# Performance work log

Measured on AMD Instinct MI355X. Metric: run time of the kernel, lower is better.

The kernel has to match this reference:

```python
import jax, jax.numpy as jnp
import numpy as np

D = 2048
N_DRUG, N_PROT = 10000, 20000
E = 100000


def setup_inputs() -> dict:
    key = jax.random.key(0)
    ks = jax.random.split(key, 10)
    return {
        "x_drug": jax.random.normal(ks[0], (N_DRUG, D), dtype=jnp.float32),
        "x_protein": jax.random.normal(ks[1], (N_PROT, D), dtype=jnp.float32),
        "rel_ddi": jax.random.normal(ks[2], (D,), dtype=jnp.float32),
        "rel_dpi": jax.random.normal(ks[3], (D,), dtype=jnp.float32),
        "ddi_src": jax.random.randint(ks[4], (E,), 0, N_DRUG, dtype=jnp.int64 if jax.config.jax_enable_x64 else jnp.int32),
        "ddi_dst": jax.random.randint(ks[5], (E,), 0, N_DRUG, dtype=jnp.int64 if jax.config.jax_enable_x64 else jnp.int32),
        "dpi_src": jax.random.randint(ks[6], (E,), 0, N_DRUG, dtype=jnp.int64 if jax.config.jax_enable_x64 else jnp.int32),
        "dpi_dst": jax.random.randint(ks[7], (E,), 0, N_PROT, dtype=jnp.int64 if jax.config.jax_enable_x64 else jnp.int32),
        "ppi_src": jax.random.randint(ks[8], (E,), 0, N_PROT, dtype=jnp.int64 if jax.config.jax_enable_x64 else jnp.int32),
        "ppi_dst": jax.random.randint(ks[9], (E,), 0, N_PROT, dtype=jnp.int64 if jax.config.jax_enable_x64 else jnp.int32),
    }


def _edge_score(x_src, x_dst, src, dst, rel):
    # gather [E, D] head/tail, DistMult-style multiply-reduce, clamp to [0, 1]
    head = x_src[src]
    tail = x_dst[dst]
    score = jnp.sum(head * rel * tail, axis=-1)
    return jnp.clip(score, 0.0, 1.0)


def reference(x_drug, x_protein, rel_ddi, rel_dpi,
              ddi_src, ddi_dst, dpi_src, dpi_dst, ppi_src, ppi_dst):
    score_ddi = _edge_score(x_drug, x_drug, ddi_src, ddi_dst, rel_ddi)
    score_dpi = _edge_score(x_drug, x_protein, dpi_src, dpi_dst, rel_dpi)
    # NOTE: original module (faithfully) applies the DPI relation to PPI edges
    score_ppi = _edge_score(x_protein, x_protein, ppi_src, ppi_dst, rel_dpi)
    return (score_ddi, score_dpi, score_ppi)
```

## Files before the change

kernel.cpp:

```cpp
#include <hip/hip_runtime.h>

#define D4 512
#define K_EDGES 32


__global__ void zero_ints(int* __restrict__ p, int n) {
    int i = blockIdx.x * blockDim.x + threadIdx.x;
    if (i < n) p[i] = 0;
}

__global__ void hist3(const int* __restrict__ s0, const int* __restrict__ s1,
                      const int* __restrict__ s2, int E,
                      int* __restrict__ cnt, int O1, int O2) {
    int i = blockIdx.x * blockDim.x + threadIdx.x;
    const int total = 3 * E;
    for (; i < total; i += gridDim.x * blockDim.x) {
        if (i < E)           atomicAdd(&cnt[s0[i]], 1);
        else if (i < 2 * E)  atomicAdd(&cnt[O1 + s1[i - E]], 1);
        else                 atomicAdd(&cnt[O2 + s2[i - 2 * E]], 1);
    }
}

__global__ void alloc3(const int* __restrict__ cnt, int* __restrict__ base,
                       int* __restrict__ cursors, int O1, int O2, int CBp) {
    int i = blockIdx.x * blockDim.x + threadIdx.x;
    if (i >= CBp) return;
    const int lane = threadIdx.x & 63;
    const int rel = (i >= O2) ? 2 : (i >= O1) ? 1 : 0;
    int c = cnt[i];
    int x = c;
#pragma unroll
    for (int d = 1; d < 64; d <<= 1) {
        int y = __shfl_up(x, d, 64);
        if (lane >= d) x += y;
    }
    int tot = __shfl(x, 63);
    int wb = 0;
    if (lane == 63) wb = atomicAdd(&cursors[rel], tot);
    wb = __shfl(wb, 63);
    base[i] = wb + x - c;
}

__global__ void scatter3(const int* __restrict__ s0, const int* __restrict__ d0_,
                         const int* __restrict__ s1, const int* __restrict__ d1_,
                         const int* __restrict__ s2, const int* __restrict__ d2_,
                         int E, int* __restrict__ base, int O1, int O2,
                         int* __restrict__ sorted, int* __restrict__ sd) {
    int i = blockIdx.x * blockDim.x + threadIdx.x;
    const int total = 3 * E;
    for (; i < total; i += gridDim.x * blockDim.x) {
        if (i < E) {
            int s = s0[i], d = d0_[i];
            int p = atomicAdd(&base[s], 1);
            sorted[p] = i; sd[p] = (s << 16) | d;
        } else if (i < 2 * E) {
            int k = i - E; int s = s1[k], d = d1_[k];
            int p = atomicAdd(&base[O1 + s], 1);
            sorted[E + p] = k; sd[E + p] = (s << 16) | d;
        } else {
            int k = i - 2 * E; int s = s2[k], d = d2_[k];
            int p = atomicAdd(&base[O2 + s], 1);
            sorted[2 * E + p] = k; sd[2 * E + p] = (s << 16) | d;
        }
    }
}

__global__ __launch_bounds__(256, 4) void score_sorted(
    const float4* __restrict__ xdrug, const float4* __restrict__ xprot,
    const float4* __restrict__ rddi,  const float4* __restrict__ rdpi,
    const int* __restrict__ sorted, const int* __restrict__ sd,
    int* __restrict__ queue, float* __restrict__ out, int E)
{
    const int lane = threadIdx.x & 63;
    const int wpb = blockDim.x >> 6;
    const int wid = blockIdx.x * wpb + (threadIdx.x >> 6);
    const int nw = gridDim.x * wpb;
    const int cpr = (E + K_EDGES - 1) / K_EDGES;
    const int total_chunks = 3 * cpr;

    int c = wid;
    while (c < total_chunks) {
        const int r = (c >= 2 * cpr) ? 2 : (c >= cpr) ? 1 : 0;
        const int ci = c - r * cpr;
        const int e_lo = ci * K_EDGES;
        const int n = min(K_EDGES, E - e_lo);

        const float4 *xs, *xd, *rel;
        if (r == 0)      { xs = xdrug; xd = xdrug; rel = rddi; }
        else if (r == 1) { xs = xdrug; xd = xprot; rel = rdpi; }
        else             { xs = xprot; xd = xprot; rel = rdpi; }
        const int* sl  = sorted + (size_t)r * E + e_lo;
        const int* sdl = sd     + (size_t)r * E + e_lo;
        float* o = out + (size_t)r * E;

        int eL = 0, sdL = 0;
        if (lane < n) { eL = sl[lane]; sdL = sdl[lane]; }

        float4 hr[8], tA[8], tB[8];
        int cur = -1;

        {
            int sd0 = __shfl(sdL, 0);
            const float4* tp = xd + (size_t)(sd0 & 0xffff) * D4;
#pragma unroll
            for (int j = 0; j < 8; ++j) tA[j] = tp[j * 64 + lane];
        }

        for (int i = 0; i < n; i += 2) {
            if (i + 1 < n) {
                int sdn = __shfl(sdL, i + 1);
                const float4* tq = xd + (size_t)(sdn & 0xffff) * D4;
#pragma unroll
                for (int j = 0; j < 8; ++j) tB[j] = tq[j * 64 + lane];
            }
            {
                int sdi = __shfl(sdL, i);
                int s = sdi >> 16;
                if (s != cur) {
                    cur = s;
                    const float4* hp = xs + (size_t)s * D4;
#pragma unroll
                    for (int j = 0; j < 8; ++j) {
                        float4 h = hp[j * 64 + lane], rv = rel[j * 64 + lane];
                        hr[j].x = h.x * rv.x; hr[j].y = h.y * rv.y;
                        hr[j].z = h.z * rv.z; hr[j].w = h.w * rv.w;
                    }
                }
                float acc = 0.f;
#pragma unroll
                for (int j = 0; j < 8; ++j) {
                    acc = fmaf(hr[j].x, tA[j].x, acc);
                    acc = fmaf(hr[j].y, tA[j].y, acc);
                    acc = fmaf(hr[j].z, tA[j].z, acc);
                    acc = fmaf(hr[j].w, tA[j].w, acc);
                }
#pragma unroll
                for (int off = 32; off; off >>= 1) acc += __shfl_down(acc, off, 64);
                int e = __shfl(eL, i);
                if (lane == 0) o[e] = fminf(fmaxf(acc, 0.f), 1.f);
            }
            if (i + 1 >= n) break;
            if (i + 2 < n) {
                int sdn = __shfl(sdL, i + 2);
                const float4* tq = xd + (size_t)(sdn & 0xffff) * D4;
#pragma unroll
                for (int j = 0; j < 8; ++j) tA[j] = tq[j * 64 + lane];
            }
            {
                int sdi = __shfl(sdL, i + 1);
                int s = sdi >> 16;
                if (s != cur) {
                    cur = s;
                    const float4* hp = xs + (size_t)s * D4;
#pragma unroll
                    for (int j = 0; j < 8; ++j) {
                        float4 h = hp[j * 64 + lane], rv = rel[j * 64 + lane];
                        hr[j].x = h.x * rv.x; hr[j].y = h.y * rv.y;
                        hr[j].z = h.z * rv.z; hr[j].w = h.w * rv.w;
                    }
                }
                float acc = 0.f;
#pragma unroll
                for (int j = 0; j < 8; ++j) {
                    acc = fmaf(hr[j].x, tB[j].x, acc);
                    acc = fmaf(hr[j].y, tB[j].y, acc);
                    acc = fmaf(hr[j].z, tB[j].z, acc);
                    acc = fmaf(hr[j].w, tB[j].w, acc);
                }
#pragma unroll
                for (int off = 32; off; off >>= 1) acc += __shfl_down(acc, off, 64);
                int e = __shfl(eL, i + 1);
                if (lane == 0) o[e] = fminf(fmaxf(acc, 0.f), 1.f);
            }
        }

        int nc = 0;
        if (lane == 0) nc = atomicAdd(queue, 1);
        c = nw + __shfl(nc, 0);
    }
}

__global__ __launch_bounds__(256) void edge_score_all(
    const float4* __restrict__ xdrug, const float4* __restrict__ xprot,
    const float4* __restrict__ rddi,  const float4* __restrict__ rdpi,
    const int* __restrict__ ddi_src, const int* __restrict__ ddi_dst,
    const int* __restrict__ dpi_src, const int* __restrict__ dpi_dst,
    const int* __restrict__ ppi_src, const int* __restrict__ ppi_dst,
    float* __restrict__ out, int E)
{
    __shared__ float4 srel[2][D4];
    for (int i = threadIdx.x; i < D4; i += blockDim.x) {
        srel[0][i] = rddi[i];
        srel[1][i] = rdpi[i];
    }
    __syncthreads();
    const int lane = threadIdx.x & 63;
    const int wpb = blockDim.x >> 6;
    int wid = blockIdx.x * wpb + (threadIdx.x >> 6);
    const int nw = gridDim.x * wpb;
    const int total = 3 * E;
    for (int e = wid; e < total; e += nw) {
        const float4 *hp, *tp;
        int sel;
        if (e < E)          { hp = xdrug + (size_t)ddi_src[e] * D4; tp = xdrug + (size_t)ddi_dst[e] * D4; sel = 0; }
        else if (e < 2 * E) { int k = e - E;     hp = xdrug + (size_t)dpi_src[k] * D4; tp = xprot + (size_t)dpi_dst[k] * D4; sel = 1; }
        else                { int k = e - 2 * E; hp = xprot + (size_t)ppi_src[k] * D4; tp = xprot + (size_t)ppi_dst[k] * D4; sel = 1; }
        float acc = 0.f;
#pragma unroll
        for (int j = 0; j < 8; ++j) {
            const int idx = j * 64 + lane;
            float4 h = hp[idx], t = tp[idx], rr = srel[sel][idx];
            acc = fmaf(h.x * rr.x, t.x, acc);
            acc = fmaf(h.y * rr.y, t.y, acc);
            acc = fmaf(h.z * rr.z, t.z, acc);
            acc = fmaf(h.w * rr.w, t.w, acc);
        }
#pragma unroll
        for (int off = 32; off; off >>= 1) acc += __shfl_down(acc, off, 64);
        if (lane == 0) out[e] = fminf(fmaxf(acc, 0.f), 1.f);
    }
}

extern "C" void kernel_launch(void* const* d_in, const int* in_sizes, int n_in,
                              void* d_out, int out_size, void* d_ws, size_t ws_size,
                              hipStream_t stream) {
    const float* x_drug    = (const float*)d_in[0];
    const float* x_protein = (const float*)d_in[1];
    const float* rel_ddi   = (const float*)d_in[2];
    const float* rel_dpi   = (const float*)d_in[3];
    const int* ddi_src = (const int*)d_in[4];
    const int* ddi_dst = (const int*)d_in[5];
    const int* dpi_src = (const int*)d_in[6];
    const int* dpi_dst = (const int*)d_in[7];
    const int* ppi_src = (const int*)d_in[8];
    const int* ppi_dst = (const int*)d_in[9];

    const int D  = in_sizes[2];
    const int nd = in_sizes[0] / D;
    const int np = in_sizes[1] / D;
    const int E  = in_sizes[4];
    float* out = (float*)d_out;

    const int ndp = ((nd + 63) / 64) * 64;
    const int npp = ((np + 63) / 64) * 64;
    const int O1  = ndp;
    const int O2  = ndp + ndp;
    const int CBp = O2 + npp;

    const size_t need = (size_t)(2 * CBp + 8 + 6 * E) * sizeof(int);

    if (ws_size < need) {
        edge_score_all<<<2048, 256, 0, stream>>>(
            (const float4*)x_drug, (const float4*)x_protein,
            (const float4*)rel_ddi, (const float4*)rel_dpi,
            ddi_src, ddi_dst, dpi_src, dpi_dst, ppi_src, ppi_dst, out, E);
        return;
    }

    int* cnt    = (int*)d_ws;
    int* aux    = cnt + CBp;
    int* base   = aux + 8;
    int* sorted = base + CBp;
    int* sd     = sorted + 3 * E;

    zero_ints<<<(CBp + 8 + 255) / 256, 256, 0, stream>>>(cnt, CBp + 8);
    hist3<<<1024, 256, 0, stream>>>(ddi_src, dpi_src, ppi_src, E, cnt, O1, O2);
    alloc3<<<(CBp + 255) / 256, 256, 0, stream>>>(cnt, base, aux, O1, O2, CBp);
    scatter3<<<1024, 256, 0, stream>>>(ddi_src, ddi_dst, dpi_src, dpi_dst,
                                       ppi_src, ppi_dst, E, base, O1, O2, sorted, sd);

    score_sorted<<<1024, 256, 0, stream>>>(
        (const float4*)x_drug, (const float4*)x_protein,
        (const float4*)rel_ddi, (const float4*)rel_dpi,
        sorted, sd, aux + 3, out, E);
}
```

Baseline: 708.6 us.

## Split edge buckets by destination half to localize tail-row gathers

Measured after the change: 761.9 us. 7.5% more time.

```diff
diff --git a/kernel.cpp b/kernel.cpp
--- a/kernel.cpp
+++ b/kernel.cpp
@@ -9,24 +9,31 @@
     if (i < n) p[i] = 0;
 }
 
-__global__ void hist3(const int* __restrict__ s0, const int* __restrict__ s1,
-                      const int* __restrict__ s2, int E,
-                      int* __restrict__ cnt, int O1, int O2) {
+__global__ void hist3(const int* __restrict__ s0, const int* __restrict__ d0_,
+                      const int* __restrict__ s1, const int* __restrict__ d1_,
+                      const int* __restrict__ s2, const int* __restrict__ d2_,
+                      int E, int* __restrict__ cnt,
+                      int ndp, int npp, int hd, int hp) {
     int i = blockIdx.x * blockDim.x + threadIdx.x;
     const int total = 3 * E;
     for (; i < total; i += gridDim.x * blockDim.x) {
-        if (i < E)           atomicAdd(&cnt[s0[i]], 1);
-        else if (i < 2 * E)  atomicAdd(&cnt[O1 + s1[i - E]], 1);
-        else                 atomicAdd(&cnt[O2 + s2[i - 2 * E]], 1);
+        int b;
+        if (i < E)           { b = (d0_[i] < hd ? 0 : ndp) + s0[i]; }
+        else if (i < 2 * E)  { int k = i - E;     b = 2 * ndp + (d1_[k] < hp ? 0 : ndp) + s1[k]; }
+        else                 { int k = i - 2 * E; b = 4 * ndp + (d2_[k] < hp ? 0 : npp) + s2[k]; }
+        atomicAdd(&cnt[b], 1);
     }
 }
 
 __global__ void alloc3(const int* __restrict__ cnt, int* __restrict__ base,
-                       int* __restrict__ cursors, int O1, int O2, int CBp) {
+                       int* __restrict__ cursors, int ndp, int npp, int E, int CBp) {
     int i = blockIdx.x * blockDim.x + threadIdx.x;
     if (i >= CBp) return;
     const int lane = threadIdx.x & 63;
-    const int rel = (i >= O2) ? 2 : (i >= O1) ? 1 : 0;
+    int g;
+    if (i < 2 * ndp)      g = (i < ndp) ? 0 : 1;
+    else if (i < 4 * ndp) g = (i < 3 * ndp) ? 2 : 3;
+    else                  g = (i < 4 * ndp + npp) ? 4 : 5;
     int c = cnt[i];
     int x = c;
 #pragma unroll
@@ -36,36 +43,43 @@
     }
     int tot = __shfl(x, 63);
     int wb = 0;
-    if (lane == 63) wb = atomicAdd(&cursors[rel], tot);
+    if (lane == 63) wb = atomicAdd(&cursors[g], tot);
     wb = __shfl(wb, 63);
-    base[i] = wb + x - c;
+    int ex = wb + x - c;
+    base[i] = (g & 1) ? (E - ex - c) : ex;
 }
 
 __global__ void scatter3(const int* __restrict__ s0, const int* __restrict__ d0_,
                          const int* __restrict__ s1, const int* __restrict__ d1_,
                          const int* __restrict__ s2, const int* __restrict__ d2_,
-                         int E, int* __restrict__ base, int O1, int O2,
+                         int E, int* __restrict__ base, int ndp, int npp,
+                         int hd, int hp,
                          int* __restrict__ sorted, int* __restrict__ sd) {
     int i = blockIdx.x * blockDim.x + threadIdx.x;
     const int total = 3 * E;
     for (; i < total; i += gridDim.x * blockDim.x) {
         if (i < E) {
             int s = s0[i], d = d0_[i];
-            int p = atomicAdd(&base[s], 1);
+            int b = (d < hd ? 0 : ndp) + s;
+            int p = atomicAdd(&base[b], 1);
             sorted[p] = i; sd[p] = (s << 16) | d;
         } else if (i < 2 * E) {
             int k = i - E; int s = s1[k], d = d1_[k];
-            int p = atomicAdd(&base[O1 + s], 1);
+            int b = 2 * ndp + (d < hp ? 0 : ndp) + s;
+            int p = atomicAdd(&base[b], 1);
             sorted[E + p] = k; sd[E + p] = (s << 16) | d;
         } else {
             int k = i - 2 * E; int s = s2[k], d = d2_[k];
-            int p = atomicAdd(&base[O2 + s], 1);
+            int b = 4 * ndp + (d < hp ? 0 : npp) + s;
+            int p = atomicAdd(&base[b], 1);
             sorted[2 * E + p] = k; sd[2 * E + p] = (s << 16) | d;
         }
     }
 }
 
-__global__ __launch_bounds__(256, 4) void score_sorted(
+__global__ __launch_bounds__(256)
+__attribute__((amdgpu_waves_per_eu(4, 4)))
+void score_sorted(
     const float4* __restrict__ xdrug, const float4* __restrict__ xprot,
     const float4* __restrict__ rddi,  const float4* __restrict__ rdpi,
     const int* __restrict__ sorted, const int* __restrict__ sd,
@@ -126,14 +140,15 @@
                         hr[j].z = h.z * rv.z; hr[j].w = h.w * rv.w;
                     }
                 }
-                float acc = 0.f;
+                float a0 = 0.f, a1 = 0.f, a2 = 0.f, a3 = 0.f;
 #pragma unroll
                 for (int j = 0; j < 8; ++j) {
-                    acc = fmaf(hr[j].x, tA[j].x, acc);
-                    acc = fmaf(hr[j].y, tA[j].y, acc);
-                    acc = fmaf(hr[j].z, tA[j].z, acc);
-                    acc = fmaf(hr[j].w, tA[j].w, acc);
-                }
+                    a0 = fmaf(hr[j].x, tA[j].x, a0);
+                    a1 = fmaf(hr[j].y, tA[j].y, a1);
+                    a2 = fmaf(hr[j].z, tA[j].z, a2);
+                    a3 = fmaf(hr[j].w, tA[j].w, a3);
+                }
+                float acc = (a0 + a1) + (a2 + a3);
 #pragma unroll
                 for (int off = 32; off; off >>= 1) acc += __shfl_down(acc, off, 64);
                 int e = __shfl(eL, i);
@@ -159,14 +174,15 @@
                         hr[j].z = h.z * rv.z; hr[j].w = h.w * rv.w;
                     }
                 }
-                float acc = 0.f;
+                float a0 = 0.f, a1 = 0.f, a2 = 0.f, a3 = 0.f;
 #pragma unroll
                 for (int j = 0; j < 8; ++j) {
-                    acc = fmaf(hr[j].x, tB[j].x, acc);
-                    acc = fmaf(hr[j].y, tB[j].y, acc);
-                    acc = fmaf(hr[j].z, tB[j].z, acc);
-                    acc = fmaf(hr[j].w, tB[j].w, acc);
-                }
+                    a0 = fmaf(hr[j].x, tB[j].x, a0);
+                    a1 = fmaf(hr[j].y, tB[j].y, a1);
+                    a2 = fmaf(hr[j].z, tB[j].z, a2);
+                    a3 = fmaf(hr[j].w, tB[j].w, a3);
+                }
+                float acc = (a0 + a1) + (a2 + a3);
 #pragma unroll
                 for (int off = 32; off; off >>= 1) acc += __shfl_down(acc, off, 64);
                 int e = __shfl(eL, i + 1);
@@ -243,11 +259,11 @@
 
     const int ndp = ((nd + 63) / 64) * 64;
     const int npp = ((np + 63) / 64) * 64;
-    const int O1  = ndp;
-    const int O2  = ndp + ndp;
-    const int CBp = O2 + npp;
-
-    const size_t need = (size_t)(2 * CBp + 8 + 6 * E) * sizeof(int);
+    const int CBp = 4 * ndp + 2 * npp;
+    const int hd  = nd >> 1;
+    const int hp  = np >> 1;
+
+    const size_t need = (size_t)(2 * CBp + 16 + 6 * E) * sizeof(int);
 
     if (ws_size < need) {
         edge_score_all<<<2048, 256, 0, stream>>>(
@@ -259,18 +275,20 @@
 
     int* cnt    = (int*)d_ws;
     int* aux    = cnt + CBp;
-    int* base   = aux + 8;
+    int* base   = aux + 16;
     int* sorted = base + CBp;
     int* sd     = sorted + 3 * E;
 
-    zero_ints<<<(CBp + 8 + 255) / 256, 256, 0, stream>>>(cnt, CBp + 8);
-    hist3<<<1024, 256, 0, stream>>>(ddi_src, dpi_src, ppi_src, E, cnt, O1, O2);
-    alloc3<<<(CBp + 255) / 256, 256, 0, stream>>>(cnt, base, aux, O1, O2, CBp);
-    scatter3<<<1024, 256, 0, stream>>>(ddi_src, ddi_dst, dpi_src, dpi_dst,
-                                       ppi_src, ppi_dst, E, base, O1, O2, sorted, sd);
+    zero_ints<<<(CBp + 16 + 255) / 256, 256, 0, stream>>>(cnt, CBp + 16);
+    hist3<<<2048, 256, 0, stream>>>(ddi_src, ddi_dst, dpi_src, dpi_dst,
+                                    ppi_src, ppi_dst, E, cnt, ndp, npp, hd, hp);
+    alloc3<<<(CBp + 255) / 256, 256, 0, stream>>>(cnt, base, aux, ndp, npp, E, CBp);
+    scatter3<<<2048, 256, 0, stream>>>(ddi_src, ddi_dst, dpi_src, dpi_dst,
+                                       ppi_src, ppi_dst, E, base, ndp, npp,
+                                       hd, hp, sorted, sd);
 
     score_sorted<<<1024, 256, 0, stream>>>(
         (const float4*)x_drug, (const float4*)x_protein,
         (const float4*)rel_ddi, (const float4*)rel_dpi,
-        sorted, sd, aux + 3, out, E);
-}
+        sorted, sd, aux + 8, out, E);
+}
```

## Gather fp16 rel-premultiplied tail tables and refine near-boundary scores in fp32

Applied to the files above, without the earlier changes.

New measurement: 624.2 us. 11.9% less time.

```diff
diff --git a/kernel.cpp b/kernel.cpp
--- a/kernel.cpp
+++ b/kernel.cpp
@@ -1,8 +1,28 @@
 #include <hip/hip_runtime.h>
+#include <hip/hip_fp16.h>
 
 #define D4 512
-#define K_EDGES 32
-
+#define T4 256
+#define K_EDGES 16
+
+__global__ __launch_bounds__(256) void cvt16(
+    const float4* __restrict__ xd, const float4* __restrict__ xp,
+    const float4* __restrict__ rddi, const float4* __restrict__ rdpi,
+    __half* __restrict__ drug16, __half* __restrict__ prot16,
+    int nd4, int np4)
+{
+    int i = blockIdx.x * blockDim.x + threadIdx.x;
+    const int total = nd4 + np4;
+    for (; i < total; i += gridDim.x * blockDim.x) {
+        float4 v, r; __half* o; int idx;
+        if (i < nd4) { v = xd[i];          r = rddi[i & 511]; o = drug16; idx = i; }
+        else { int k = i - nd4; v = xp[k]; r = rdpi[k & 511]; o = prot16; idx = k; }
+        __half2 h01 = __floats2half2_rn(v.x * r.x, v.y * r.y);
+        __half2 h23 = __floats2half2_rn(v.z * r.z, v.w * r.w);
+        uint2 pk = make_uint2(*(const unsigned*)&h01, *(const unsigned*)&h23);
+        ((uint2*)o)[idx] = pk;
+    }
+}
 
 __global__ void zero_ints(int* __restrict__ p, int n) {
     int i = blockIdx.x * blockDim.x + threadIdx.x;
@@ -11,22 +31,22 @@
 
 __global__ void hist3(const int* __restrict__ s0, const int* __restrict__ s1,
                       const int* __restrict__ s2, int E,
-                      int* __restrict__ cnt, int O1, int O2) {
+                      int* __restrict__ cnt, int ndp) {
     int i = blockIdx.x * blockDim.x + threadIdx.x;
     const int total = 3 * E;
     for (; i < total; i += gridDim.x * blockDim.x) {
         if (i < E)           atomicAdd(&cnt[s0[i]], 1);
-        else if (i < 2 * E)  atomicAdd(&cnt[O1 + s1[i - E]], 1);
-        else                 atomicAdd(&cnt[O2 + s2[i - 2 * E]], 1);
+        else if (i < 2 * E)  atomicAdd(&cnt[ndp + s1[i - E]], 1);
+        else                 atomicAdd(&cnt[2 * ndp + s2[i - 2 * E]], 1);
     }
 }
 
 __global__ void alloc3(const int* __restrict__ cnt, int* __restrict__ base,
-                       int* __restrict__ cursors, int O1, int O2, int CBp) {
-    int i = blockIdx.x * blockDim.x + threadIdx.x;
-    if (i >= CBp) return;
-    const int lane = threadIdx.x & 63;
-    const int rel = (i >= O2) ? 2 : (i >= O1) ? 1 : 0;
+                       int* __restrict__ cursors, int ndp, int CB) {
+    int i = blockIdx.x * blockDim.x + threadIdx.x;
+    if (i >= CB) return;
+    const int lane = threadIdx.x & 63;
+    const int g = (i < ndp) ? 0 : (i < 2 * ndp) ? 1 : 2;
     int c = cnt[i];
     int x = c;
 #pragma unroll
@@ -36,7 +56,7 @@
     }
     int tot = __shfl(x, 63);
     int wb = 0;
-    if (lane == 63) wb = atomicAdd(&cursors[rel], tot);
+    if (lane == 63) wb = atomicAdd(&cursors[g], tot);
     wb = __shfl(wb, 63);
     base[i] = wb + x - c;
 }
@@ -44,7 +64,7 @@
 __global__ void scatter3(const int* __restrict__ s0, const int* __restrict__ d0_,
                          const int* __restrict__ s1, const int* __restrict__ d1_,
                          const int* __restrict__ s2, const int* __restrict__ d2_,
-                         int E, int* __restrict__ base, int O1, int O2,
+                         int E, int* __restrict__ base, int ndp,
                          int* __restrict__ sorted, int* __restrict__ sd) {
     int i = blockIdx.x * blockDim.x + threadIdx.x;
     const int total = 3 * E;
@@ -55,21 +75,22 @@
             sorted[p] = i; sd[p] = (s << 16) | d;
         } else if (i < 2 * E) {
             int k = i - E; int s = s1[k], d = d1_[k];
-            int p = atomicAdd(&base[O1 + s], 1);
+            int p = atomicAdd(&base[ndp + s], 1);
             sorted[E + p] = k; sd[E + p] = (s << 16) | d;
         } else {
             int k = i - 2 * E; int s = s2[k], d = d2_[k];
-            int p = atomicAdd(&base[O2 + s], 1);
+            int p = atomicAdd(&base[2 * ndp + s], 1);
             sorted[2 * E + p] = k; sd[2 * E + p] = (s << 16) | d;
         }
     }
 }
 
-__global__ __launch_bounds__(256, 4) void score_sorted(
+__global__ __launch_bounds__(256) void score16(
     const float4* __restrict__ xdrug, const float4* __restrict__ xprot,
-    const float4* __restrict__ rddi,  const float4* __restrict__ rdpi,
+    const float4* __restrict__ drug16, const float4* __restrict__ prot16,
     const int* __restrict__ sorted, const int* __restrict__ sd,
-    int* __restrict__ queue, float* __restrict__ out, int E)
+    int* __restrict__ refine, int* __restrict__ rcnt,
+    float* __restrict__ out, int E)
 {
     const int lane = threadIdx.x & 63;
     const int wpb = blockDim.x >> 6;
@@ -78,8 +99,122 @@
     const int cpr = (E + K_EDGES - 1) / K_EDGES;
     const int total_chunks = 3 * cpr;
 
-    int c = wid;
-    while (c < total_chunks) {
+    for (int c = wid; c < total_chunks; c += nw) {
+        const int r = (c >= 2 * cpr) ? 2 : (c >= cpr) ? 1 : 0;
+        const int ci = c - r * cpr;
+        const int e_lo = ci * K_EDGES;
+        const int n = min(K_EDGES, E - e_lo);
+
+        const float4* xs = (r < 2) ? xdrug : xprot;
+        const float4* xt = (r == 0) ? drug16 : prot16;
+        const int* sl  = sorted + (size_t)r * E + e_lo;
+        const int* sdl = sd     + (size_t)r * E + e_lo;
+        float* o = out + (size_t)r * E;
+
+        int eL = 0, sdL = 0;
+        if (lane < n) { eL = sl[lane]; sdL = sdl[lane]; }
+
+        float4 hr[8];
+        int cur = -1;
+
+        for (int i = 0; i < n; ++i) {
+            const int sdi = __shfl(sdL, i);
+            const int e   = __shfl(eL, i);
+            const int s = sdi >> 16;
+            if (s != cur) {
+                cur = s;
+                const float4* hp = xs + (size_t)s * D4;
+#pragma unroll
+                for (int g = 0; g < 4; ++g) {
+                    hr[2 * g]     = hp[2 * (g * 64 + lane)];
+                    hr[2 * g + 1] = hp[2 * (g * 64 + lane) + 1];
+                }
+            }
+            const float4* tq = xt + (size_t)(sdi & 0xffff) * T4;
+            float a0 = 0.f, a1 = 0.f, a2 = 0.f, a3 = 0.f;
+#pragma unroll
+            for (int g = 0; g < 4; ++g) {
+                float4 tv = tq[g * 64 + lane];
+                const __half2* t2 = (const __half2*)&tv;
+                float2 f0 = __half22float2(t2[0]);
+                float2 f1 = __half22float2(t2[1]);
+                float2 f2 = __half22float2(t2[2]);
+                float2 f3 = __half22float2(t2[3]);
+                a0 = fmaf(hr[2 * g].x, f0.x, a0);
+                a1 = fmaf(hr[2 * g].y, f0.y, a1);
+                a2 = fmaf(hr[2 * g].z, f1.x, a2);
+                a3 = fmaf(hr[2 * g].w, f1.y, a3);
+                a0 = fmaf(hr[2 * g + 1].x, f2.x, a0);
+                a1 = fmaf(hr[2 * g + 1].y, f2.y, a1);
+                a2 = fmaf(hr[2 * g + 1].z, f3.x, a2);
+                a3 = fmaf(hr[2 * g + 1].w, f3.y, a3);
+            }
+            float acc = (a0 + a1) + (a2 + a3);
+#pragma unroll
+            for (int off = 32; off; off >>= 1) acc += __shfl_down(acc, off, 64);
+            if (lane == 0) {
+                o[e] = fminf(fmaxf(acc, 0.f), 1.f);
+                if (acc > -1.5f && acc < 2.5f) {
+                    int p = atomicAdd(rcnt, 1);
+                    refine[p] = (r << 20) | e;
+                }
+            }
+        }
+    }
+}
+
+__global__ __launch_bounds__(256) void refine_f32(
+    const float4* __restrict__ xdrug, const float4* __restrict__ xprot,
+    const float4* __restrict__ rddi,  const float4* __restrict__ rdpi,
+    const int* __restrict__ ddi_src, const int* __restrict__ ddi_dst,
+    const int* __restrict__ dpi_src, const int* __restrict__ dpi_dst,
+    const int* __restrict__ ppi_src, const int* __restrict__ ppi_dst,
+    const int* __restrict__ refine, const int* __restrict__ rcnt,
+    float* __restrict__ out, int E)
+{
+    const int lane = threadIdx.x & 63;
+    const int wpb = blockDim.x >> 6;
+    const int wid = blockIdx.x * wpb + (threadIdx.x >> 6);
+    const int nw = gridDim.x * wpb;
+    const int count = rcnt[0];
+    for (int k = wid; k < count; k += nw) {
+        const int pe = refine[k];
+        const int r = pe >> 20, e = pe & 0xFFFFF;
+        const float4 *hp, *tp, *rel;
+        if (r == 0)      { hp = xdrug + (size_t)ddi_src[e] * D4; tp = xdrug + (size_t)ddi_dst[e] * D4; rel = rddi; }
+        else if (r == 1) { hp = xdrug + (size_t)dpi_src[e] * D4; tp = xprot + (size_t)dpi_dst[e] * D4; rel = rdpi; }
+        else             { hp = xprot + (size_t)ppi_src[e] * D4; tp = xprot + (size_t)ppi_dst[e] * D4; rel = rdpi; }
+        float a0 = 0.f, a1 = 0.f, a2 = 0.f, a3 = 0.f;
+#pragma unroll
+        for (int j = 0; j < 8; ++j) {
+            const int idx = j * 64 + lane;
+            float4 h = hp[idx], t = tp[idx], rv = rel[idx];
+            a0 = fmaf(h.x * rv.x, t.x, a0);
+            a1 = fmaf(h.y * rv.y, t.y, a1);
+            a2 = fmaf(h.z * rv.z, t.z, a2);
+            a3 = fmaf(h.w * rv.w, t.w, a3);
+        }
+        float acc = (a0 + a1) + (a2 + a3);
+#pragma unroll
+        for (int off = 32; off; off >>= 1) acc += __shfl_down(acc, off, 64);
+        if (lane == 0) out[(size_t)r * E + e] = fminf(fmaxf(acc, 0.f), 1.f);
+    }
+}
+
+__global__ __launch_bounds__(256) void score_f32(
+    const float4* __restrict__ xdrug, const float4* __restrict__ xprot,
+    const float4* __restrict__ rddi,  const float4* __restrict__ rdpi,
+    const int* __restrict__ sorted, const int* __restrict__ sd,
+    float* __restrict__ out, int E)
+{
+    const int lane = threadIdx.x & 63;
+    const int wpb = blockDim.x >> 6;
+    const int wid = blockIdx.x * wpb + (threadIdx.x >> 6);
+    const int nw = gridDim.x * wpb;
+    const int cpr = (E + K_EDGES - 1) / K_EDGES;
+    const int total_chunks = 3 * cpr;
+
+    for (int c = wid; c < total_chunks; c += nw) {
         const int r = (c >= 2 * cpr) ? 2 : (c >= cpr) ? 1 : 0;
         const int ci = c - r * cpr;
         const int e_lo = ci * K_EDGES;
@@ -93,90 +228,36 @@
         const int* sdl = sd     + (size_t)r * E + e_lo;
         float* o = out + (size_t)r * E;
 
-        int eL = 0, sdL = 0;
-        if (lane < n) { eL = sl[lane]; sdL = sdl[lane]; }
-
-        float4 hr[8], tA[8], tB[8];
+        float4 hr[8];
         int cur = -1;
-
-        {
-            int sd0 = __shfl(sdL, 0);
-            const float4* tp = xd + (size_t)(sd0 & 0xffff) * D4;
-#pragma unroll
-            for (int j = 0; j < 8; ++j) tA[j] = tp[j * 64 + lane];
-        }
-
-        for (int i = 0; i < n; i += 2) {
-            if (i + 1 < n) {
-                int sdn = __shfl(sdL, i + 1);
-                const float4* tq = xd + (size_t)(sdn & 0xffff) * D4;
-#pragma unroll
-                for (int j = 0; j < 8; ++j) tB[j] = tq[j * 64 + lane];
-            }
-            {
-                int sdi = __shfl(sdL, i);
-                int s = sdi >> 16;
-                if (s != cur) {
-                    cur = s;
-                    const float4* hp = xs + (size_t)s * D4;
-#pragma unroll
-                    for (int j = 0; j < 8; ++j) {
-                        float4 h = hp[j * 64 + lane], rv = rel[j * 64 + lane];
-                        hr[j].x = h.x * rv.x; hr[j].y = h.y * rv.y;
-                        hr[j].z = h.z * rv.z; hr[j].w = h.w * rv.w;
-                    }
+        for (int i = 0; i < n; ++i) {
+            const int e = sl[i];
+            const int sdi = sdl[i];
+            const int s = sdi >> 16;
+            if (s != cur) {
+                cur = s;
+                const float4* hp = xs + (size_t)s * D4;
+#pragma unroll
+                for (int j = 0; j < 8; ++j) {
+                    float4 h = hp[j * 64 + lane], rv = rel[j * 64 + lane];
+                    hr[j].x = h.x * rv.x; hr[j].y = h.y * rv.y;
+                    hr[j].z = h.z * rv.z; hr[j].w = h.w * rv.w;
                 }
-                float acc = 0.f;
-#pragma unroll
-                for (int j = 0; j < 8; ++j) {
-                    acc = fmaf(hr[j].x, tA[j].x, acc);
-                    acc = fmaf(hr[j].y, tA[j].y, acc);
-                    acc = fmaf(hr[j].z, tA[j].z, acc);
-                    acc = fmaf(hr[j].w, tA[j].w, acc);
-                }
-#pragma unroll
-                for (int off = 32; off; off >>= 1) acc += __shfl_down(acc, off, 64);
-                int e = __shfl(eL, i);
-                if (lane == 0) o[e] = fminf(fmaxf(acc, 0.f), 1.f);
-            }
-            if (i + 1 >= n) break;
-            if (i + 2 < n) {
-                int sdn = __shfl(sdL, i + 2);
-                const float4* tq = xd + (size_t)(sdn & 0xffff) * D4;
-#pragma unroll
-                for (int j = 0; j < 8; ++j) tA[j] = tq[j * 64 + lane];
-            }
-            {
-                int sdi = __shfl(sdL, i + 1);
-                int s = sdi >> 16;
-                if (s != cur) {
-                    cur = s;
-                    const float4* hp = xs + (size_t)s * D4;
-#pragma unroll
-                    for (int j = 0; j < 8; ++j) {
-                        float4 h = hp[j * 64 + lane], rv = rel[j * 64 + lane];
-                        hr[j].x = h.x * rv.x; hr[j].y = h.y * rv.y;
-                        hr[j].z = h.z * rv.z; hr[j].w = h.w * rv.w;
-                    }
-                }
-                float acc = 0.f;
-#pragma unroll
-                for (int j = 0; j < 8; ++j) {
-                    acc = fmaf(hr[j].x, tB[j].x, acc);
-                    acc = fmaf(hr[j].y, tB[j].y, acc);
-                    acc = fmaf(hr[j].z, tB[j].z, acc);
-                    acc = fmaf(hr[j].w, tB[j].w, acc);
-                }
-#pragma unroll
-                for (int off = 32; off; off >>= 1) acc += __shfl_down(acc, off, 64);
-                int e = __shfl(eL, i + 1);
-                if (lane == 0) o[e] = fminf(fmaxf(acc, 0.f), 1.f);
-            }
-        }
-
-        int nc = 0;
-        if (lane == 0) nc = atomicAdd(queue, 1);
-        c = nw + __shfl(nc, 0);
+            }
+            const float4* tp = xd + (size_t)(sdi & 0xffff) * D4;
+            float acc = 0.f;
+#pragma unroll
+            for (int j = 0; j < 8; ++j) {
+                float4 t = tp[j * 64 + lane];
+                acc = fmaf(hr[j].x, t.x, acc);
+                acc = fmaf(hr[j].y, t.y, acc);
+                acc = fmaf(hr[j].z, t.z, acc);
+                acc = fmaf(hr[j].w, t.w, acc);
+            }
+#pragma unroll
+            for (int off = 32; off; off >>= 1) acc += __shfl_down(acc, off, 64);
+            if (lane == 0) o[e] = fminf(fmaxf(acc, 0.f), 1.f);
+        }
     }
 }
 
@@ -243,13 +324,15 @@
 
     const int ndp = ((nd + 63) / 64) * 64;
     const int npp = ((np + 63) / 64) * 64;
-    const int O1  = ndp;
-    const int O2  = ndp + ndp;
-    const int CBp = O2 + npp;
-
-    const size_t need = (size_t)(2 * CBp + 8 + 6 * E) * sizeof(int);
-
-    if (ws_size < need) {
+    const int CB  = 2 * ndp + npp;
+
+    const size_t b_d16 = (size_t)nd * D * 2;
+    const size_t b_p16 = (size_t)np * D * 2;
+    const size_t ints_sort = (size_t)(2 * CB + 16 + 6 * E) * sizeof(int);
+    const size_t need_sort = ints_sort;
+    const size_t need_full = b_d16 + b_p16 + ints_sort + (size_t)3 * E * sizeof(int);
+
+    if (ws_size < need_sort) {
         edge_score_all<<<2048, 256, 0, stream>>>(
             (const float4*)x_drug, (const float4*)x_protein,
             (const float4*)rel_ddi, (const float4*)rel_dpi,
@@ -257,20 +340,46 @@
         return;
     }
 
-    int* cnt    = (int*)d_ws;
-    int* aux    = cnt + CBp;
-    int* base   = aux + 8;
-    int* sorted = base + CBp;
+    const bool full = (ws_size >= need_full);
+    char* wp = (char*)d_ws;
+    __half* drug16 = nullptr; __half* prot16 = nullptr;
+    if (full) {
+        drug16 = (__half*)wp;  wp += b_d16;
+        prot16 = (__half*)wp;  wp += b_p16;
+    }
+    int* cnt    = (int*)wp;
+    int* aux    = cnt + CB;
+    int* base   = aux + 16;
+    int* sorted = base + CB;
     int* sd     = sorted + 3 * E;
-
-    zero_ints<<<(CBp + 8 + 255) / 256, 256, 0, stream>>>(cnt, CBp + 8);
-    hist3<<<1024, 256, 0, stream>>>(ddi_src, dpi_src, ppi_src, E, cnt, O1, O2);
-    alloc3<<<(CBp + 255) / 256, 256, 0, stream>>>(cnt, base, aux, O1, O2, CBp);
+    int* refine = sd + 3 * E;
+
+    if (full)
+        cvt16<<<2048, 256, 0, stream>>>(
+            (const float4*)x_drug, (const float4*)x_protein,
+            (const float4*)rel_ddi, (const float4*)rel_dpi,
+            drug16, prot16, nd * (D / 4), np * (D / 4));
+
+    zero_ints<<<(CB + 16 + 255) / 256, 256, 0, stream>>>(cnt, CB + 16);
+    hist3<<<1024, 256, 0, stream>>>(ddi_src, dpi_src, ppi_src, E, cnt, ndp);
+    alloc3<<<(CB + 255) / 256, 256, 0, stream>>>(cnt, base, aux, ndp, CB);
     scatter3<<<1024, 256, 0, stream>>>(ddi_src, ddi_dst, dpi_src, dpi_dst,
-                                       ppi_src, ppi_dst, E, base, O1, O2, sorted, sd);
-
-    score_sorted<<<1024, 256, 0, stream>>>(
-        (const float4*)x_drug, (const float4*)x_protein,
-        (const float4*)rel_ddi, (const float4*)rel_dpi,
-        sorted, sd, aux + 3, out, E);
-}
+                                       ppi_src, ppi_dst, E, base, ndp, sorted, sd);
+
+    if (full) {
+        score16<<<2048, 256, 0, stream>>>(
+            (const float4*)x_drug, (const float4*)x_protein,
+            (const float4*)drug16, (const float4*)prot16,
+            sorted, sd, refine, aux + 8, out, E);
+        refine_f32<<<1024, 256, 0, stream>>>(
+            (const float4*)x_drug, (const float4*)x_protein,
+            (const float4*)rel_ddi, (const float4*)rel_dpi,
+            ddi_src, ddi_dst, dpi_src, dpi_dst, ppi_src, ppi_dst,
+            refine, aux + 8, out, E);
+    } else {
+        score_f32<<<2048, 256, 0, stream>>>(
+            (const float4*)x_drug, (const float4*)x_protein,
+            (const float4*)rel_ddi, (const float4*)rel_dpi,
+            sorted, sd, out, E);
+    }
+}
```
